# Performance work log

Hardware: AMD Instinct MI355X
Metric: run time of the kernel (lower is better)

Reference implementation:

```python
import jax, jax.numpy as jnp
import numpy as np

N = 100000      # nodes
E = 1600000     # edges
NFEAT = 128
NHID = 32
NHEADS = 8
NCLASS = 40
K = 2           # hop_num
BETA = 0.1      # diffusion teleport weight
ALPHA = 0.2     # leaky relu slope


def setup_inputs() -> dict:
    key = jax.random.key(0)
    ks = jax.random.split(key, 8)
    x = jax.random.normal(ks[0], (N, NFEAT), dtype=jnp.float32)
    edge_index = jax.random.randint(ks[1], (2, E), 0, N, dtype=jnp.int64)
    W = jax.random.normal(ks[2], (NHEADS, NFEAT, NHID), dtype=jnp.float32) * 0.1
    a_src = jax.random.normal(ks[3], (NHEADS, NHID), dtype=jnp.float32) * 0.1
    a_dst = jax.random.normal(ks[4], (NHEADS, NHID), dtype=jnp.float32) * 0.1
    W_out = jax.random.normal(ks[5], (NHEADS * NHID, NCLASS), dtype=jnp.float32) * 0.1
    a_src_out = jax.random.normal(ks[6], (NCLASS,), dtype=jnp.float32) * 0.1
    a_dst_out = jax.random.normal(ks[7], (NCLASS,), dtype=jnp.float32) * 0.1
    return {"x": x, "edge_index": edge_index, "W": W, "a_src": a_src,
            "a_dst": a_dst, "W_out": W_out, "a_src_out": a_src_out,
            "a_dst_out": a_dst_out}


def _khop_attention(h0, src, dst, a_s, a_d):
    """One sparse k-hop attention head. h0: [N, D] transformed features."""
    s = h0 @ a_s            # [N]
    t = h0 @ a_d            # [N]
    e = jax.nn.leaky_relu(s[src] + t[dst], ALPHA)          # [E]
    # numerically stable per-destination softmax over incoming edges
    m = jax.ops.segment_max(e, dst, num_segments=N)        # [N]
    m = jnp.where(jnp.isfinite(m), m, 0.0)                 # empty segments -> -inf
    p = jnp.exp(e - m[dst])                                # [E]
    denom = jax.ops.segment_sum(p, dst, num_segments=N) + 1e-16
    w = p / denom[dst]                                     # [E] attention coeffs
    # k-hop decaying diffusion: feat <- (1-beta)*A_att feat + beta*h0
    feat = h0
    for _ in range(K):
        msg = jax.ops.segment_sum(w[:, None] * feat[src], dst, num_segments=N)
        feat = (1.0 - BETA) * msg + BETA * h0
    return feat


def reference(x, edge_index, W, a_src, a_dst, W_out, a_src_out, a_dst_out):
    src, dst = edge_index[0], edge_index[1]
    # multi-head layer (concat=True -> elu per head, concat along features)
    heads = [jax.nn.elu(_khop_attention(x @ W[i], src, dst, a_src[i], a_dst[i]))
             for i in range(NHEADS)]
    h = jnp.concatenate(heads, axis=1)                     # [N, NHEADS*NHID]
    # output attention layer (concat=False -> raw output)
    out = _khop_attention(h @ W_out, src, dst, a_src_out, a_dst_out)  # [N, NCLASS]
    return jax.nn.log_softmax(jax.nn.elu(out), axis=1)
```

## Files before the change

kernel.cpp:

```cpp
#include <hip/hip_runtime.h>
#include <hip/hip_fp16.h>
#include <stdint.h>

#define NN      100000
#define EE      1600000
#define NFEATC  128
#define NHIDC   32
#define NHEADSC 8
#define NCLASSC 40
#define FDIM    256
#define NBLK    ((NN+255)/256)

typedef unsigned short u16;
typedef __attribute__((ext_vector_type(8))) short bf16x8;
typedef __attribute__((ext_vector_type(4))) float f32x4;

__device__ __forceinline__ float b2f(u16 u){ union{uint32_t i; float f;} v; v.i=((uint32_t)u)<<16; return v.f; }
__device__ __forceinline__ float lof(uint32_t u){ union{uint32_t i; float f;} v; v.i=u<<16; return v.f; }
__device__ __forceinline__ float hif(uint32_t u){ union{uint32_t i; float f;} v; v.i=u&0xFFFF0000u; return v.f; }
__device__ __forceinline__ u16 f2b(float f){ union{float f; uint32_t i;} v; v.f=f; uint32_t x=v.i; return (u16)((x + 0x7FFFu + ((x>>16)&1u))>>16); }
__device__ __forceinline__ uint32_t pack2(float a, float b){ return (uint32_t)f2b(a) | ((uint32_t)f2b(b)<<16); }
__device__ __forceinline__ float lrelu(float e){ return e > 0.f ? e : 0.2f*e; }

__global__ __launch_bounds__(256) void k_transposeW(const float* __restrict__ W, u16* __restrict__ Wt){
  int i = blockIdx.x*256 + threadIdx.x;
  if (i >= FDIM*NFEATC) return;
  int c = i >> 7, k = i & 127;
  int head = c >> 5, hid = c & 31;
  Wt[c*NFEATC + k] = f2b(W[head*(NFEATC*NHIDC) + k*NHIDC + hid]);
}

__global__ __launch_bounds__(256) void k_gemm1_mfma(const float* __restrict__ x, const u16* __restrict__ Wt,
                                                    u16* __restrict__ h0){
  int w = threadIdx.x >> 6, lane = threadIdx.x & 63;
  int nt = blockIdx.x;
  int m = lane & 15, q = lane >> 4;
  int row = nt*16 + m;
  int c0 = w*64;
  const float* xrow = x + (size_t)row*NFEATC;
  f32x4 acc0 = {0.f,0.f,0.f,0.f}, acc1 = {0.f,0.f,0.f,0.f};
  f32x4 acc2 = {0.f,0.f,0.f,0.f}, acc3 = {0.f,0.f,0.f,0.f};
  #pragma unroll
  for (int kk=0; kk<NFEATC; kk+=32){
    int ko = kk + q*8;
    float4 xa = *(const float4*)(xrow + ko);
    float4 xb = *(const float4*)(xrow + ko + 4);
    bf16x8 a;
    a[0]=(short)f2b(xa.x); a[1]=(short)f2b(xa.y); a[2]=(short)f2b(xa.z); a[3]=(short)f2b(xa.w);
    a[4]=(short)f2b(xb.x); a[5]=(short)f2b(xb.y); a[6]=(short)f2b(xb.z); a[7]=(short)f2b(xb.w);
    bf16x8 b0 = *(const bf16x8*)(Wt + (size_t)(c0 +  0 + m)*NFEATC + ko);
    bf16x8 b1 = *(const bf16x8*)(Wt + (size_t)(c0 + 16 + m)*NFEATC + ko);
    bf16x8 b2 = *(const bf16x8*)(Wt + (size_t)(c0 + 32 + m)*NFEATC + ko);
    bf16x8 b3 = *(const bf16x8*)(Wt + (size_t)(c0 + 48 + m)*NFEATC + ko);
    acc0 = __builtin_amdgcn_mfma_f32_16x16x32_bf16(a, b0, acc0, 0,0,0);
    acc1 = __builtin_amdgcn_mfma_f32_16x16x32_bf16(a, b1, acc1, 0,0,0);
    acc2 = __builtin_amdgcn_mfma_f32_16x16x32_bf16(a, b2, acc2, 0,0,0);
    acc3 = __builtin_amdgcn_mfma_f32_16x16x32_bf16(a, b3, acc3, 0,0,0);
  }
  #pragma unroll
  for (int r=0; r<4; r++){
    size_t base = (size_t)(nt*16 + q*4 + r)*FDIM + c0 + m;
    h0[base +  0] = f2b(acc0[r]);
    h0[base + 16] = f2b(acc1[r]);
    h0[base + 32] = f2b(acc2[r]);
    h0[base + 48] = f2b(acc3[r]);
  }
}

__global__ __launch_bounds__(256) void k_st(const u16* __restrict__ h0, const float* __restrict__ a_src,
                                            const float* __restrict__ a_dst, u16* __restrict__ s,
                                            u16* __restrict__ t_){
  int i = blockIdx.x*256 + threadIdx.x;
  if (i >= NN*NHEADSC) return;
  int n = i>>3, head = i&7;
  const u16* hp = h0 + (size_t)n*FDIM + head*NHIDC;
  const float* ap = a_src + head*NHIDC;
  const float* bp = a_dst + head*NHIDC;
  float ss=0.f, tt=0.f;
  #pragma unroll
  for (int j=0;j<NHIDC;j++){
    float h = b2f(hp[j]);
    ss = fmaf(h, ap[j], ss); tt = fmaf(h, bp[j], tt);
  }
  s[i]=f2b(ss); t_[i]=f2b(tt);
}

__global__ __launch_bounds__(256) void k_zero(int* __restrict__ p, int n){
  int i = blockIdx.x*256 + threadIdx.x;
  if (i < n) p[i] = 0;
}
__global__ __launch_bounds__(256) void k_zero_f(float* __restrict__ p, int n){
  int i = blockIdx.x*256 + threadIdx.x;
  if (i < n) p[i] = 0.f;
}
__global__ __launch_bounds__(256) void k_count(const int* __restrict__ dst, int* __restrict__ counts){
  int e = blockIdx.x*256 + threadIdx.x;
  if (e < EE) atomicAdd(&counts[dst[e]], 1);
}
__global__ __launch_bounds__(256) void k_blocksum(const int* __restrict__ counts, int* __restrict__ bsum){
  __shared__ int wsum[4];
  int b = blockIdx.x, t = threadIdx.x;
  int i = b*256 + t;
  int v = (i < NN) ? counts[i] : 0;
  #pragma unroll
  for (int off=32; off; off>>=1) v += __shfl_xor(v, off);
  if ((t & 63) == 0) wsum[t>>6] = v;
  __syncthreads();
  if (t == 0) bsum[b] = wsum[0]+wsum[1]+wsum[2]+wsum[3];
}
__global__ __launch_bounds__(512) void k_scan_bsum(const int* __restrict__ bsum, int* __restrict__ boff){
  __shared__ int lds[512];
  int t = threadIdx.x;
  int v = (t < NBLK) ? bsum[t] : 0;
  lds[t] = v; __syncthreads();
  for (int off=1; off<512; off<<=1){
    int u = (t>=off) ? lds[t-off] : 0;
    __syncthreads();
    lds[t] += u;
    __syncthreads();
  }
  if (t < NBLK) boff[t] = lds[t] - v;
}
__global__ __launch_bounds__(256) void k_scan_final(const int* __restrict__ counts, const int* __restrict__ boff,
                                                    int* __restrict__ row_start){
  __shared__ int lds[256];
  int b = blockIdx.x, t = threadIdx.x;
  int i = b*256 + t;
  int v = (i < NN) ? counts[i] : 0;
  lds[t] = v; __syncthreads();
  for (int off=1; off<256; off<<=1){
    int u = (t>=off) ? lds[t-off] : 0;
    __syncthreads();
    lds[t] += u;
    __syncthreads();
  }
  if (i < NN) row_start[i] = boff[b] + lds[t] - v;
  if (b == 0 && t == 0) row_start[NN] = EE;
}
__global__ __launch_bounds__(256) void k_scatter(const int* __restrict__ src, const int* __restrict__ dst,
                                                 const int* __restrict__ row_start, int* __restrict__ fill,
                                                 int* __restrict__ csr_src){
  int e = blockIdx.x*256 + threadIdx.x;
  if (e >= EE) return;
  int d = dst[e];
  int pos = row_start[d] + atomicAdd(&fill[d], 1);
  csr_src[pos] = src[e];
}

__global__ __launch_bounds__(256) void k_att(const u16* __restrict__ s, const u16* __restrict__ t_,
                                             const int* __restrict__ row_start, const int* __restrict__ csr_src,
                                             u16* __restrict__ p_all, __half* __restrict__ scale){
  int i = blockIdx.x*256 + threadIdx.x;
  if (i >= NN*NHEADSC) return;
  int n = i>>3, head = i&7;
  int beg = row_start[n], end = row_start[n+1];
  float tn = b2f(t_[i]);
  float d0=0.f,d1=0.f,d2=0.f,d3=0.f;
  int pos = beg;
  for (; pos+4<=end; pos+=4){
    int u0=csr_src[pos], u1=csr_src[pos+1], u2=csr_src[pos+2], u3=csr_src[pos+3];
    float e0=lrelu(b2f(s[u0*NHEADSC+head])+tn);
    float e1=lrelu(b2f(s[u1*NHEADSC+head])+tn);
    float e2=lrelu(b2f(s[u2*NHEADSC+head])+tn);
    float e3=lrelu(b2f(s[u3*NHEADSC+head])+tn);
    u16 p0=f2b(__expf(e0)), p1=f2b(__expf(e1)), p2=f2b(__expf(e2)), p3=f2b(__expf(e3));
    p_all[(size_t)(pos+0)*NHEADSC+head]=p0;
    p_all[(size_t)(pos+1)*NHEADSC+head]=p1;
    p_all[(size_t)(pos+2)*NHEADSC+head]=p2;
    p_all[(size_t)(pos+3)*NHEADSC+head]=p3;
    d0+=b2f(p0); d1+=b2f(p1); d2+=b2f(p2); d3+=b2f(p3);
  }
  for (; pos<end; pos++){
    int u = csr_src[pos];
    float e = lrelu(b2f(s[u*NHEADSC+head])+tn);
    u16 pb = f2b(__expf(e));
    p_all[(size_t)pos*NHEADSC+head]=pb;
    d0 += b2f(pb);
  }
  scale[i] = __float2half(1.0f/(((d0+d1)+(d2+d3)) + 1e-16f));
}

#define ACC8(p, g) \
  a0=fmaf(p,lof(g.x),a0); a1=fmaf(p,hif(g.x),a1); \
  a2=fmaf(p,lof(g.y),a2); a3=fmaf(p,hif(g.y),a3); \
  a4=fmaf(p,lof(g.z),a4); a5=fmaf(p,hif(g.z),a5); \
  a6=fmaf(p,lof(g.w),a6); a7=fmaf(p,hif(g.w),a7);

__global__ __launch_bounds__(256) void k_hop1(const u16* __restrict__ h0, const u16* __restrict__ p_all,
                                              const __half* __restrict__ scale, const int* __restrict__ row_start,
                                              const int* __restrict__ csr_src, u16* __restrict__ featA){
  int wv = threadIdx.x >> 6, l = threadIdx.x & 63;
  int n = blockIdx.x*4 + wv;
  int half = l >> 5, sl = l & 31;
  int cg = 8*sl;
  int head = sl >> 2;
  float sc_ = __half2float(scale[n*NHEADSC + head]);
  int beg = row_start[n], end = row_start[n+1];
  float a0=0.f,a1=0.f,a2=0.f,a3=0.f,a4=0.f,a5=0.f,a6=0.f,a7=0.f;
  int pos = beg;
  for (; pos+8<=end; pos+=8){
    int e0=csr_src[pos+0+half], e1=csr_src[pos+2+half], e2=csr_src[pos+4+half], e3=csr_src[pos+6+half];
    float p0=b2f(p_all[(size_t)(pos+0+half)*NHEADSC+head]);
    float p1=b2f(p_all[(size_t)(pos+2+half)*NHEADSC+head]);
    float p2=b2f(p_all[(size_t)(pos+4+half)*NHEADSC+head]);
    float p3=b2f(p_all[(size_t)(pos+6+half)*NHEADSC+head]);
    uint4 g0 = *(const uint4*)(h0 + (size_t)e0*FDIM + cg);
    uint4 g1 = *(const uint4*)(h0 + (size_t)e1*FDIM + cg);
    uint4 g2 = *(const uint4*)(h0 + (size_t)e2*FDIM + cg);
    uint4 g3 = *(const uint4*)(h0 + (size_t)e3*FDIM + cg);
    ACC8(p0, g0) ACC8(p1, g1) ACC8(p2, g2) ACC8(p3, g3)
  }
  for (; pos+2<=end; pos+=2){
    int e = csr_src[pos+half];
    float p = b2f(p_all[(size_t)(pos+half)*NHEADSC+head]);
    uint4 g = *(const uint4*)(h0 + (size_t)e*FDIM + cg);
    ACC8(p, g)
  }
  if (pos < end && half == 0){
    int e = csr_src[pos];
    float p = b2f(p_all[(size_t)pos*NHEADSC+head]);
    uint4 g = *(const uint4*)(h0 + (size_t)e*FDIM + cg);
    ACC8(p, g)
  }
  a0 += __shfl_xor(a0, 32); a1 += __shfl_xor(a1, 32);
  a2 += __shfl_xor(a2, 32); a3 += __shfl_xor(a3, 32);
  a4 += __shfl_xor(a4, 32); a5 += __shfl_xor(a5, 32);
  a6 += __shfl_xor(a6, 32); a7 += __shfl_xor(a7, 32);
  if (half == 0){
    uint4 hu = *(const uint4*)(h0 + (size_t)n*FDIM + cg);
    float r0 = 0.9f*sc_*a0 + 0.1f*lof(hu.x);
    float r1 = 0.9f*sc_*a1 + 0.1f*hif(hu.x);
    float r2 = 0.9f*sc_*a2 + 0.1f*lof(hu.y);
    float r3 = 0.9f*sc_*a3 + 0.1f*hif(hu.y);
    float r4 = 0.9f*sc_*a4 + 0.1f*lof(hu.z);
    float r5 = 0.9f*sc_*a5 + 0.1f*hif(hu.z);
    float r6 = 0.9f*sc_*a6 + 0.1f*lof(hu.w);
    float r7 = 0.9f*sc_*a7 + 0.1f*hif(hu.w);
    uint4 o;
    o.x = pack2(r0,r1); o.y = pack2(r2,r3); o.z = pack2(r4,r5); o.w = pack2(r6,r7);
    *(uint4*)(featA + (size_t)n*FDIM + cg) = o;
  }
}

__global__ __launch_bounds__(256) void k_hop2(const u16* __restrict__ featA, const u16* __restrict__ h0,
                                              const u16* __restrict__ p_all, const __half* __restrict__ scale,
                                              const int* __restrict__ row_start, const int* __restrict__ csr_src,
                                              const float* __restrict__ W_out, float* __restrict__ out0){
  __shared__ float hs[4][FDIM+4];
  int wv = threadIdx.x >> 6, l = threadIdx.x & 63;
  int n = blockIdx.x*4 + wv;
  int half = l >> 5, sl = l & 31;
  int cg = 8*sl;
  int head = sl >> 2;
  float sc_ = __half2float(scale[n*NHEADSC + head]);
  int beg = row_start[n], end = row_start[n+1];
  float a0=0.f,a1=0.f,a2=0.f,a3=0.f,a4=0.f,a5=0.f,a6=0.f,a7=0.f;
  int pos = beg;
  for (; pos+8<=end; pos+=8){
    int e0=csr_src[pos+0+half], e1=csr_src[pos+2+half], e2=csr_src[pos+4+half], e3=csr_src[pos+6+half];
    float p0=b2f(p_all[(size_t)(pos+0+half)*NHEADSC+head]);
    float p1=b2f(p_all[(size_t)(pos+2+half)*NHEADSC+head]);
    float p2=b2f(p_all[(size_t)(pos+4+half)*NHEADSC+head]);
    float p3=b2f(p_all[(size_t)(pos+6+half)*NHEADSC+head]);
    uint4 g0 = *(const uint4*)(featA + (size_t)e0*FDIM + cg);
    uint4 g1 = *(const uint4*)(featA + (size_t)e1*FDIM + cg);
    uint4 g2 = *(const uint4*)(featA + (size_t)e2*FDIM + cg);
    uint4 g3 = *(const uint4*)(featA + (size_t)e3*FDIM + cg);
    ACC8(p0, g0) ACC8(p1, g1) ACC8(p2, g2) ACC8(p3, g3)
  }
  for (; pos+2<=end; pos+=2){
    int e = csr_src[pos+half];
    float p = b2f(p_all[(size_t)(pos+half)*NHEADSC+head]);
    uint4 g = *(const uint4*)(featA + (size_t)e*FDIM + cg);
    ACC8(p, g)
  }
  if (pos < end && half == 0){
    int e = csr_src[pos];
    float p = b2f(p_all[(size_t)pos*NHEADSC+head]);
    uint4 g = *(const uint4*)(featA + (size_t)e*FDIM + cg);
    ACC8(p, g)
  }
  a0 += __shfl_xor(a0, 32); a1 += __shfl_xor(a1, 32);
  a2 += __shfl_xor(a2, 32); a3 += __shfl_xor(a3, 32);
  a4 += __shfl_xor(a4, 32); a5 += __shfl_xor(a5, 32);
  a6 += __shfl_xor(a6, 32); a7 += __shfl_xor(a7, 32);
  if (half == 0){
    uint4 hu = *(const uint4*)(h0 + (size_t)n*FDIM + cg);
    float r0 = 0.9f*sc_*a0 + 0.1f*lof(hu.x);
    float r1 = 0.9f*sc_*a1 + 0.1f*hif(hu.x);
    float r2 = 0.9f*sc_*a2 + 0.1f*lof(hu.y);
    float r3 = 0.9f*sc_*a3 + 0.1f*hif(hu.y);
    float r4 = 0.9f*sc_*a4 + 0.1f*lof(hu.z);
    float r5 = 0.9f*sc_*a5 + 0.1f*hif(hu.z);
    float r6 = 0.9f*sc_*a6 + 0.1f*lof(hu.w);
    float r7 = 0.9f*sc_*a7 + 0.1f*hif(hu.w);
    hs[wv][cg  ] = r0 > 0.f ? r0 : (__expf(r0)-1.0f);
    hs[wv][cg+1] = r1 > 0.f ? r1 : (__expf(r1)-1.0f);
    hs[wv][cg+2] = r2 > 0.f ? r2 : (__expf(r2)-1.0f);
    hs[wv][cg+3] = r3 > 0.f ? r3 : (__expf(r3)-1.0f);
    hs[wv][cg+4] = r4 > 0.f ? r4 : (__expf(r4)-1.0f);
    hs[wv][cg+5] = r5 > 0.f ? r5 : (__expf(r5)-1.0f);
    hs[wv][cg+6] = r6 > 0.f ? r6 : (__expf(r6)-1.0f);
    hs[wv][cg+7] = r7 > 0.f ? r7 : (__expf(r7)-1.0f);
  }
  __syncthreads();
  int t = threadIdx.x;
  if (t < 4*NCLASSC){
    int node = t/NCLASSC, c = t%NCLASSC;
    const float* hv = hs[node];
    const float* wp = W_out + c;
    float o = 0.f;
    #pragma unroll 8
    for (int k=0;k<FDIM;k++) o = fmaf(hv[k], wp[(size_t)k*NCLASSC], o);
    out0[(size_t)(blockIdx.x*4+node)*NCLASSC + c] = o;
  }
}

__global__ __launch_bounds__(256) void k_st_out(const float* __restrict__ out0, const float* __restrict__ a_s,
                                                const float* __restrict__ a_d, float* __restrict__ s,
                                                float* __restrict__ t_){
  int n = blockIdx.x*256 + threadIdx.x;
  if (n >= NN) return;
  const float* r = out0 + (size_t)n*NCLASSC;
  float ss=0.f, tt=0.f;
  for (int c=0;c<NCLASSC;c++){ float v=r[c]; ss=fmaf(v,a_s[c],ss); tt=fmaf(v,a_d[c],tt); }
  s[n]=ss; t_[n]=tt;
}

__global__ __launch_bounds__(256) void k_att_out(const float* __restrict__ s, const float* __restrict__ t_,
                                                 const int* __restrict__ row_start, const int* __restrict__ csr_src,
                                                 float* __restrict__ p_out, float* __restrict__ scale_out){
  int n = blockIdx.x*256 + threadIdx.x;
  if (n >= NN) return;
  int beg = row_start[n], end = row_start[n+1];
  float tn = t_[n];
  float d0=0.f,d1=0.f,d2=0.f,d3=0.f;
  int pos = beg;
  for (; pos+4<=end; pos+=4){
    int u0=csr_src[pos], u1=csr_src[pos+1], u2=csr_src[pos+2], u3=csr_src[pos+3];
    float p0=__expf(lrelu(s[u0]+tn));
    float p1=__expf(lrelu(s[u1]+tn));
    float p2=__expf(lrelu(s[u2]+tn));
    float p3=__expf(lrelu(s[u3]+tn));
    p_out[pos]=p0; p_out[pos+1]=p1; p_out[pos+2]=p2; p_out[pos+3]=p3;
    d0+=p0; d1+=p1; d2+=p2; d3+=p3;
  }
  for (; pos<end; pos++){
    float p = __expf(lrelu(s[csr_src[pos]]+tn));
    p_out[pos] = p;
    d0 += p;
  }
  scale_out[n] = 1.0f/(((d0+d1)+(d2+d3)) + 1e-16f);
}

__global__ __launch_bounds__(64) void k_hop1_out(const float* __restrict__ out0, const float* __restrict__ p_out,
                                                 const float* __restrict__ scale_out, const int* __restrict__ row_start,
                                                 const int* __restrict__ csr_src, u16* __restrict__ outA){
  int n = blockIdx.x, t = threadIdx.x;
  float sc_ = scale_out[n];
  int beg = row_start[n], end = row_start[n+1];
  int tc = (t < NCLASSC) ? t : 0;
  float a0=0.f,a1=0.f,a2=0.f,a3=0.f;
  int pos = beg;
  for (; pos+4<=end; pos+=4){
    int u0=csr_src[pos], u1=csr_src[pos+1], u2=csr_src[pos+2], u3=csr_src[pos+3];
    float p0=p_out[pos], p1=p_out[pos+1], p2=p_out[pos+2], p3=p_out[pos+3];
    float f0=out0[(size_t)u0*NCLASSC+tc];
    float f1=out0[(size_t)u1*NCLASSC+tc];
    float f2=out0[(size_t)u2*NCLASSC+tc];
    float f3=out0[(size_t)u3*NCLASSC+tc];
    a0=fmaf(p0,f0,a0); a1=fmaf(p1,f1,a1); a2=fmaf(p2,f2,a2); a3=fmaf(p3,f3,a3);
  }
  for (; pos<end; pos++){
    a0=fmaf(p_out[pos], out0[(size_t)csr_src[pos]*NCLASSC+tc], a0);
  }
  if (t < NCLASSC){
    float res = 0.9f*sc_*((a0+a1)+(a2+a3)) + 0.1f*out0[(size_t)n*NCLASSC + t];
    outA[(size_t)n*NCLASSC + t] = f2b(res);
  }
}

__global__ __launch_bounds__(64) void k_hop2_out_final(const u16* __restrict__ outA, const float* __restrict__ out0,
                                                       const float* __restrict__ p_out, const float* __restrict__ scale_out,
                                                       const int* __restrict__ row_start, const int* __restrict__ csr_src,
                                                       float* __restrict__ out){
  int n = blockIdx.x, t = threadIdx.x;
  float sc_ = scale_out[n];
  int beg = row_start[n], end = row_start[n+1];
  int tc = (t < NCLASSC) ? t : 0;
  float a0=0.f,a1=0.f,a2=0.f,a3=0.f;
  int pos = beg;
  for (; pos+4<=end; pos+=4){
    int u0=csr_src[pos], u1=csr_src[pos+1], u2=csr_src[pos+2], u3=csr_src[pos+3];
    float p0=p_out[pos], p1=p_out[pos+1], p2=p_out[pos+2], p3=p_out[pos+3];
    float f0=b2f(outA[(size_t)u0*NCLASSC+tc]);
    float f1=b2f(outA[(size_t)u1*NCLASSC+tc]);
    float f2=b2f(outA[(size_t)u2*NCLASSC+tc]);
    float f3=b2f(outA[(size_t)u3*NCLASSC+tc]);
    a0=fmaf(p0,f0,a0); a1=fmaf(p1,f1,a1); a2=fmaf(p2,f2,a2); a3=fmaf(p3,f3,a3);
  }
  for (; pos<end; pos++){
    a0=fmaf(p_out[pos], b2f(outA[(size_t)csr_src[pos]*NCLASSC+tc]), a0);
  }
  float v = -1e30f;
  if (t < NCLASSC){
    float res = 0.9f*sc_*((a0+a1)+(a2+a3)) + 0.1f*out0[(size_t)n*NCLASSC + t];
    v = res > 0.f ? res : (__expf(res)-1.0f);
  }
  float m = v;
  #pragma unroll
  for (int off=32; off; off>>=1) m = fmaxf(m, __shfl_xor(m, off));
  float ex = (t < NCLASSC) ? __expf(v - m) : 0.f;
  float ssum = ex;
  #pragma unroll
  for (int off=32; off; off>>=1) ssum += __shfl_xor(ssum, off);
  if (t < NCLASSC) out[(size_t)n*NCLASSC + t] = v - m - __logf(ssum);
}

extern "C" void kernel_launch(void* const* d_in, const int* in_sizes, int n_in,
                              void* d_out, int out_size, void* d_ws, size_t ws_size,
                              hipStream_t stream){
  const float* x        = (const float*)d_in[0];
  const int*   ei       = (const int*)d_in[1];
  const float* W        = (const float*)d_in[2];
  const float* a_src    = (const float*)d_in[3];
  const float* a_dst    = (const float*)d_in[4];
  const float* W_out    = (const float*)d_in[5];
  const float* a_src_o  = (const float*)d_in[6];
  const float* a_dst_o  = (const float*)d_in[7];
  float* out            = (float*)d_out;
  const int* e_src = ei;
  const int* e_dst = ei + EE;

  char* ws = (char*)d_ws;
  size_t off = 0;
  auto alloc = [&](size_t bytes)->char*{ char* p = ws + off; off += (bytes + 255) & ~(size_t)255; return p; };

  u16*    h0        = (u16*)   alloc((size_t)NN*FDIM*2);
  u16*    featA     = (u16*)   alloc((size_t)NN*FDIM*2);
  float*  out0      = (float*) alloc((size_t)NN*NCLASSC*4);
  int*    csr_src   = (int*)   alloc((size_t)EE*4);
  int*    row_start = (int*)   alloc((size_t)(NN+1)*4);
  char*   regS      =          alloc((size_t)NN*NHEADSC*2*2);
  u16*    p_all     = (u16*)   alloc((size_t)EE*NHEADSC*2);
  __half* scale     = (__half*)alloc((size_t)NN*NHEADSC*2);
  int*    counts    = (int*)   alloc((size_t)NN*4);
  int*    bsum      = (int*)   alloc((size_t)NBLK*4);
  int*    boff      = (int*)   alloc((size_t)NBLK*4);
  u16*    Wt        = (u16*)   alloc((size_t)FDIM*NFEATC*2);

  u16*   s         = (u16*)regS;
  u16*   t_        = (u16*)(regS + (size_t)NN*NHEADSC*2);
  float* s_out     = (float*)regS;
  float* t_out     = s_out + NN;
  float* scale_out = t_out + NN;
  u16*   outA      = (u16*)featA;
  float* p_out     = (float*)p_all;

  k_transposeW<<<(FDIM*NFEATC+255)/256, 256, 0, stream>>>(W, Wt);
  k_gemm1_mfma<<<NN/16, 256, 0, stream>>>(x, Wt, h0);
  k_st<<<(NN*NHEADSC+255)/256, 256, 0, stream>>>(h0, a_src, a_dst, s, t_);

  k_zero<<<(NN+255)/256, 256, 0, stream>>>(counts, NN);
  k_count<<<(EE+255)/256, 256, 0, stream>>>(e_dst, counts);
  k_blocksum<<<NBLK, 256, 0, stream>>>(counts, bsum);
  k_scan_bsum<<<1, 512, 0, stream>>>(bsum, boff);
  k_scan_final<<<NBLK, 256, 0, stream>>>(counts, boff, row_start);
  k_zero<<<(NN+255)/256, 256, 0, stream>>>(counts, NN);
  k_scatter<<<(EE+255)/256, 256, 0, stream>>>(e_src, e_dst, row_start, counts, csr_src);

  k_att<<<(NN*NHEADSC+255)/256, 256, 0, stream>>>(s, t_, row_start, csr_src, p_all, scale);
  k_hop1<<<NN/4, 256, 0, stream>>>(h0, p_all, scale, row_start, csr_src, featA);
  k_hop2<<<NN/4, 256, 0, stream>>>(featA, h0, p_all, scale, row_start, csr_src, W_out, out0);

  k_st_out<<<(NN+255)/256, 256, 0, stream>>>(out0, a_src_o, a_dst_o, s_out, t_out);
  k_att_out<<<(NN+255)/256, 256, 0, stream>>>(s_out, t_out, row_start, csr_src, p_out, scale_out);
  k_hop1_out<<<NN, 64, 0, stream>>>(out0, p_out, scale_out, row_start, csr_src, outA);
  k_hop2_out_final<<<NN, 64, 0, stream>>>(outA, out0, p_out, scale_out, row_start, csr_src, out);
}
```

Before: 845.5 us.

## Fuse attention softmax into hop kernels and recompute edge weights on the fly

Removes the separate attention kernels and the per-edge probability buffer. Each hop kernel now gathers s[src], recomputes the exp-leaky-relu weight, and accumulates the softmax denominator alongside the feature sum. Edge indices are software-prefetched one iteration ahead, and the remainder loops are replaced by masked lanes. W_out is pre-transposed so the dense output projection can use float4 loads. This cuts the writes and re-reads of p_all, at the cost of doing the exp twice per edge (once in each hop) plus extra small gathers of s.

```diff
diff --git a/kernel.cpp b/kernel.cpp
--- a/kernel.cpp
+++ b/kernel.cpp
@@ -28,6 +28,13 @@
   int c = i >> 7, k = i & 127;
   int head = c >> 5, hid = c & 31;
   Wt[c*NFEATC + k] = f2b(W[head*(NFEATC*NHIDC) + k*NHIDC + hid]);
+}
+
+__global__ __launch_bounds__(256) void k_transposeWout(const float* __restrict__ W_out, float* __restrict__ Wo_t){
+  int i = blockIdx.x*256 + threadIdx.x;
+  if (i >= FDIM*NCLASSC) return;
+  int c = i / FDIM, k = i % FDIM;
+  Wo_t[i] = W_out[(size_t)k*NCLASSC + c];
 }
 
 __global__ __launch_bounds__(256) void k_gemm1_mfma(const float* __restrict__ x, const u16* __restrict__ Wt,
@@ -89,10 +96,6 @@
   int i = blockIdx.x*256 + threadIdx.x;
   if (i < n) p[i] = 0;
 }
-__global__ __launch_bounds__(256) void k_zero_f(float* __restrict__ p, int n){
-  int i = blockIdx.x*256 + threadIdx.x;
-  if (i < n) p[i] = 0.f;
-}
 __global__ __launch_bounds__(256) void k_count(const int* __restrict__ dst, int* __restrict__ counts){
   int e = blockIdx.x*256 + threadIdx.x;
   if (e < EE) atomicAdd(&counts[dst[e]], 1);
@@ -147,95 +150,64 @@
   csr_src[pos] = src[e];
 }
 
-__global__ __launch_bounds__(256) void k_att(const u16* __restrict__ s, const u16* __restrict__ t_,
-                                             const int* __restrict__ row_start, const int* __restrict__ csr_src,
-                                             u16* __restrict__ p_all, __half* __restrict__ scale){
-  int i = blockIdx.x*256 + threadIdx.x;
-  if (i >= NN*NHEADSC) return;
-  int n = i>>3, head = i&7;
-  int beg = row_start[n], end = row_start[n+1];
-  float tn = b2f(t_[i]);
-  float d0=0.f,d1=0.f,d2=0.f,d3=0.f;
-  int pos = beg;
-  for (; pos+4<=end; pos+=4){
-    int u0=csr_src[pos], u1=csr_src[pos+1], u2=csr_src[pos+2], u3=csr_src[pos+3];
-    float e0=lrelu(b2f(s[u0*NHEADSC+head])+tn);
-    float e1=lrelu(b2f(s[u1*NHEADSC+head])+tn);
-    float e2=lrelu(b2f(s[u2*NHEADSC+head])+tn);
-    float e3=lrelu(b2f(s[u3*NHEADSC+head])+tn);
-    u16 p0=f2b(__expf(e0)), p1=f2b(__expf(e1)), p2=f2b(__expf(e2)), p3=f2b(__expf(e3));
-    p_all[(size_t)(pos+0)*NHEADSC+head]=p0;
-    p_all[(size_t)(pos+1)*NHEADSC+head]=p1;
-    p_all[(size_t)(pos+2)*NHEADSC+head]=p2;
-    p_all[(size_t)(pos+3)*NHEADSC+head]=p3;
-    d0+=b2f(p0); d1+=b2f(p1); d2+=b2f(p2); d3+=b2f(p3);
-  }
-  for (; pos<end; pos++){
-    int u = csr_src[pos];
-    float e = lrelu(b2f(s[u*NHEADSC+head])+tn);
-    u16 pb = f2b(__expf(e));
-    p_all[(size_t)pos*NHEADSC+head]=pb;
-    d0 += b2f(pb);
-  }
-  scale[i] = __float2half(1.0f/(((d0+d1)+(d2+d3)) + 1e-16f));
-}
-
 #define ACC8(p, g) \
   a0=fmaf(p,lof(g.x),a0); a1=fmaf(p,hif(g.x),a1); \
   a2=fmaf(p,lof(g.y),a2); a3=fmaf(p,hif(g.y),a3); \
   a4=fmaf(p,lof(g.z),a4); a5=fmaf(p,hif(g.z),a5); \
   a6=fmaf(p,lof(g.w),a6); a7=fmaf(p,hif(g.w),a7);
 
-__global__ __launch_bounds__(256) void k_hop1(const u16* __restrict__ h0, const u16* __restrict__ p_all,
-                                              const __half* __restrict__ scale, const int* __restrict__ row_start,
+__global__ __launch_bounds__(256) void k_hop1(const u16* __restrict__ h0, const u16* __restrict__ s,
+                                              const u16* __restrict__ t_, const int* __restrict__ row_start,
                                               const int* __restrict__ csr_src, u16* __restrict__ featA){
   int wv = threadIdx.x >> 6, l = threadIdx.x & 63;
   int n = blockIdx.x*4 + wv;
   int half = l >> 5, sl = l & 31;
   int cg = 8*sl;
   int head = sl >> 2;
-  float sc_ = __half2float(scale[n*NHEADSC + head]);
+  float tn = b2f(t_[n*NHEADSC + head]);
   int beg = row_start[n], end = row_start[n+1];
-  float a0=0.f,a1=0.f,a2=0.f,a3=0.f,a4=0.f,a5=0.f,a6=0.f,a7=0.f;
-  int pos = beg;
-  for (; pos+8<=end; pos+=8){
-    int e0=csr_src[pos+0+half], e1=csr_src[pos+2+half], e2=csr_src[pos+4+half], e3=csr_src[pos+6+half];
-    float p0=b2f(p_all[(size_t)(pos+0+half)*NHEADSC+head]);
-    float p1=b2f(p_all[(size_t)(pos+2+half)*NHEADSC+head]);
-    float p2=b2f(p_all[(size_t)(pos+4+half)*NHEADSC+head]);
-    float p3=b2f(p_all[(size_t)(pos+6+half)*NHEADSC+head]);
+  float a0=0.f,a1=0.f,a2=0.f,a3=0.f,a4=0.f,a5=0.f,a6=0.f,a7=0.f,den=0.f;
+  int e0,e1,e2,e3;
+  {
+    int v0=beg+half, v1=beg+2+half, v2=beg+4+half, v3=beg+6+half;
+    int c0=csr_src[v0<EE?v0:EE-1], c1=csr_src[v1<EE?v1:EE-1];
+    int c2=csr_src[v2<EE?v2:EE-1], c3=csr_src[v3<EE?v3:EE-1];
+    e0 = v0<end?c0:n; e1 = v1<end?c1:n; e2 = v2<end?c2:n; e3 = v3<end?c3:n;
+  }
+  for (int pos=beg; pos<end; pos+=8){
+    int w0=pos+8+half, w1=pos+10+half, w2=pos+12+half, w3=pos+14+half;
+    int c0=csr_src[w0<EE?w0:EE-1], c1=csr_src[w1<EE?w1:EE-1];
+    int c2=csr_src[w2<EE?w2:EE-1], c3=csr_src[w3<EE?w3:EE-1];
+    float s0=b2f(s[e0*NHEADSC+head]), s1=b2f(s[e1*NHEADSC+head]);
+    float s2=b2f(s[e2*NHEADSC+head]), s3=b2f(s[e3*NHEADSC+head]);
     uint4 g0 = *(const uint4*)(h0 + (size_t)e0*FDIM + cg);
     uint4 g1 = *(const uint4*)(h0 + (size_t)e1*FDIM + cg);
     uint4 g2 = *(const uint4*)(h0 + (size_t)e2*FDIM + cg);
     uint4 g3 = *(const uint4*)(h0 + (size_t)e3*FDIM + cg);
-    ACC8(p0, g0) ACC8(p1, g1) ACC8(p2, g2) ACC8(p3, g3)
-  }
-  for (; pos+2<=end; pos+=2){
-    int e = csr_src[pos+half];
-    float p = b2f(p_all[(size_t)(pos+half)*NHEADSC+head]);
-    uint4 g = *(const uint4*)(h0 + (size_t)e*FDIM + cg);
-    ACC8(p, g)
-  }
-  if (pos < end && half == 0){
-    int e = csr_src[pos];
-    float p = b2f(p_all[(size_t)pos*NHEADSC+head]);
-    uint4 g = *(const uint4*)(h0 + (size_t)e*FDIM + cg);
-    ACC8(p, g)
+    float p0 = (pos+half   < end) ? __expf(lrelu(s0+tn)) : 0.f;
+    float p1 = (pos+2+half < end) ? __expf(lrelu(s1+tn)) : 0.f;
+    float p2 = (pos+4+half < end) ? __expf(lrelu(s2+tn)) : 0.f;
+    float p3 = (pos+6+half < end) ? __expf(lrelu(s3+tn)) : 0.f;
+    den += (p0+p1)+(p2+p3);
+    ACC8(p0,g0) ACC8(p1,g1) ACC8(p2,g2) ACC8(p3,g3)
+    e0 = w0<end?c0:n; e1 = w1<end?c1:n; e2 = w2<end?c2:n; e3 = w3<end?c3:n;
   }
   a0 += __shfl_xor(a0, 32); a1 += __shfl_xor(a1, 32);
   a2 += __shfl_xor(a2, 32); a3 += __shfl_xor(a3, 32);
   a4 += __shfl_xor(a4, 32); a5 += __shfl_xor(a5, 32);
   a6 += __shfl_xor(a6, 32); a7 += __shfl_xor(a7, 32);
+  den += __shfl_xor(den, 32);
+  float sc_ = 0.9f/(den + 1e-16f);
   if (half == 0){
     uint4 hu = *(const uint4*)(h0 + (size_t)n*FDIM + cg);
-    float r0 = 0.9f*sc_*a0 + 0.1f*lof(hu.x);
-    float r1 = 0.9f*sc_*a1 + 0.1f*hif(hu.x);
-    float r2 = 0.9f*sc_*a2 + 0.1f*lof(hu.y);
-    float r3 = 0.9f*sc_*a3 + 0.1f*hif(hu.y);
-    float r4 = 0.9f*sc_*a4 + 0.1f*lof(hu.z);
-    float r5 = 0.9f*sc_*a5 + 0.1f*hif(hu.z);
-    float r6 = 0.9f*sc_*a6 + 0.1f*lof(hu.w);
-    float r7 = 0.9f*sc_*a7 + 0.1f*hif(hu.w);
+    float r0 = sc_*a0 + 0.1f*lof(hu.x);
+    float r1 = sc_*a1 + 0.1f*hif(hu.x);
+    float r2 = sc_*a2 + 0.1f*lof(hu.y);
+    float r3 = sc_*a3 + 0.1f*hif(hu.y);
+    float r4 = sc_*a4 + 0.1f*lof(hu.z);
+    float r5 = sc_*a5 + 0.1f*hif(hu.z);
+    float r6 = sc_*a6 + 0.1f*lof(hu.w);
+    float r7 = sc_*a7 + 0.1f*hif(hu.w);
     uint4 o;
     o.x = pack2(r0,r1); o.y = pack2(r2,r3); o.z = pack2(r4,r5); o.w = pack2(r6,r7);
     *(uint4*)(featA + (size_t)n*FDIM + cg) = o;
@@ -243,76 +215,86 @@
 }
 
 __global__ __launch_bounds__(256) void k_hop2(const u16* __restrict__ featA, const u16* __restrict__ h0,
-                                              const u16* __restrict__ p_all, const __half* __restrict__ scale,
+                                              const u16* __restrict__ s, const u16* __restrict__ t_,
                                               const int* __restrict__ row_start, const int* __restrict__ csr_src,
-                                              const float* __restrict__ W_out, float* __restrict__ out0){
-  __shared__ float hs[4][FDIM+4];
+                                              const float* __restrict__ Wo_t, float* __restrict__ out0){
+  __shared__ __align__(16) float hs[4][FDIM+4];
   int wv = threadIdx.x >> 6, l = threadIdx.x & 63;
   int n = blockIdx.x*4 + wv;
   int half = l >> 5, sl = l & 31;
   int cg = 8*sl;
   int head = sl >> 2;
-  float sc_ = __half2float(scale[n*NHEADSC + head]);
+  float tn = b2f(t_[n*NHEADSC + head]);
   int beg = row_start[n], end = row_start[n+1];
-  float a0=0.f,a1=0.f,a2=0.f,a3=0.f,a4=0.f,a5=0.f,a6=0.f,a7=0.f;
-  int pos = beg;
-  for (; pos+8<=end; pos+=8){
-    int e0=csr_src[pos+0+half], e1=csr_src[pos+2+half], e2=csr_src[pos+4+half], e3=csr_src[pos+6+half];
-    float p0=b2f(p_all[(size_t)(pos+0+half)*NHEADSC+head]);
-    float p1=b2f(p_all[(size_t)(pos+2+half)*NHEADSC+head]);
-    float p2=b2f(p_all[(size_t)(pos+4+half)*NHEADSC+head]);
-    float p3=b2f(p_all[(size_t)(pos+6+half)*NHEADSC+head]);
+  float a0=0.f,a1=0.f,a2=0.f,a3=0.f,a4=0.f,a5=0.f,a6=0.f,a7=0.f,den=0.f;
+  int e0,e1,e2,e3;
+  {
+    int v0=beg+half, v1=beg+2+half, v2=beg+4+half, v3=beg+6+half;
+    int c0=csr_src[v0<EE?v0:EE-1], c1=csr_src[v1<EE?v1:EE-1];
+    int c2=csr_src[v2<EE?v2:EE-1], c3=csr_src[v3<EE?v3:EE-1];
+    e0 = v0<end?c0:n; e1 = v1<end?c1:n; e2 = v2<end?c2:n; e3 = v3<end?c3:n;
+  }
+  for (int pos=beg; pos<end; pos+=8){
+    int w0=pos+8+half, w1=pos+10+half, w2=pos+12+half, w3=pos+14+half;
+    int c0=csr_src[w0<EE?w0:EE-1], c1=csr_src[w1<EE?w1:EE-1];
+    int c2=csr_src[w2<EE?w2:EE-1], c3=csr_src[w3<EE?w3:EE-1];
+    float s0=b2f(s[e0*NHEADSC+head]), s1=b2f(s[e1*NHEADSC+head]);
+    float s2=b2f(s[e2*NHEADSC+head]), s3=b2f(s[e3*NHEADSC+head]);
     uint4 g0 = *(const uint4*)(featA + (size_t)e0*FDIM + cg);
     uint4 g1 = *(const uint4*)(featA + (size_t)e1*FDIM + cg);
     uint4 g2 = *(const uint4*)(featA + (size_t)e2*FDIM + cg);
     uint4 g3 = *(const uint4*)(featA + (size_t)e3*FDIM + cg);
-    ACC8(p0, g0) ACC8(p1, g1) ACC8(p2, g2) ACC8(p3, g3)
-  }
-  for (; pos+2<=end; pos+=2){
-    int e = csr_src[pos+half];
-    float p = b2f(p_all[(size_t)(pos+half)*NHEADSC+head]);
-    uint4 g = *(const uint4*)(featA + (size_t)e*FDIM + cg);
-    ACC8(p, g)
-  }
-  if (pos < end && half == 0){
-    int e = csr_src[pos];
-    float p = b2f(p_all[(size_t)pos*NHEADSC+head]);
-    uint4 g = *(const uint4*)(featA + (size_t)e*FDIM + cg);
-    ACC8(p, g)
+    float p0 = (pos+half   < end) ? __expf(lrelu(s0+tn)) : 0.f;
+    float p1 = (pos+2+half < end) ? __expf(lrelu(s1+tn)) : 0.f;
+    float p2 = (pos+4+half < end) ? __expf(lrelu(s2+tn)) : 0.f;
+    float p3 = (pos+6+half < end) ? __expf(lrelu(s3+tn)) : 0.f;
+    den += (p0+p1)+(p2+p3);
+    ACC8(p0,g0) ACC8(p1,g1) ACC8(p2,g2) ACC8(p3,g3)
+    e0 = w0<end?c0:n; e1 = w1<end?c1:n; e2 = w2<end?c2:n; e3 = w3<end?c3:n;
   }
   a0 += __shfl_xor(a0, 32); a1 += __shfl_xor(a1, 32);
   a2 += __shfl_xor(a2, 32); a3 += __shfl_xor(a3, 32);
   a4 += __shfl_xor(a4, 32); a5 += __shfl_xor(a5, 32);
   a6 += __shfl_xor(a6, 32); a7 += __shfl_xor(a7, 32);
+  den += __shfl_xor(den, 32);
+  float sc_ = 0.9f/(den + 1e-16f);
   if (half == 0){
     uint4 hu = *(const uint4*)(h0 + (size_t)n*FDIM + cg);
-    float r0 = 0.9f*sc_*a0 + 0.1f*lof(hu.x);
-    float r1 = 0.9f*sc_*a1 + 0.1f*hif(hu.x);
-    float r2 = 0.9f*sc_*a2 + 0.1f*lof(hu.y);
-    float r3 = 0.9f*sc_*a3 + 0.1f*hif(hu.y);
-    float r4 = 0.9f*sc_*a4 + 0.1f*lof(hu.z);
-    float r5 = 0.9f*sc_*a5 + 0.1f*hif(hu.z);
-    float r6 = 0.9f*sc_*a6 + 0.1f*lof(hu.w);
-    float r7 = 0.9f*sc_*a7 + 0.1f*hif(hu.w);
-    hs[wv][cg  ] = r0 > 0.f ? r0 : (__expf(r0)-1.0f);
-    hs[wv][cg+1] = r1 > 0.f ? r1 : (__expf(r1)-1.0f);
-    hs[wv][cg+2] = r2 > 0.f ? r2 : (__expf(r2)-1.0f);
-    hs[wv][cg+3] = r3 > 0.f ? r3 : (__expf(r3)-1.0f);
-    hs[wv][cg+4] = r4 > 0.f ? r4 : (__expf(r4)-1.0f);
-    hs[wv][cg+5] = r5 > 0.f ? r5 : (__expf(r5)-1.0f);
-    hs[wv][cg+6] = r6 > 0.f ? r6 : (__expf(r6)-1.0f);
-    hs[wv][cg+7] = r7 > 0.f ? r7 : (__expf(r7)-1.0f);
+    float r0 = sc_*a0 + 0.1f*lof(hu.x);
+    float r1 = sc_*a1 + 0.1f*hif(hu.x);
+    float r2 = sc_*a2 + 0.1f*lof(hu.y);
+    float r3 = sc_*a3 + 0.1f*hif(hu.y);
+    float r4 = sc_*a4 + 0.1f*lof(hu.z);
+    float r5 = sc_*a5 + 0.1f*hif(hu.z);
+    float r6 = sc_*a6 + 0.1f*lof(hu.w);
+    float r7 = sc_*a7 + 0.1f*hif(hu.w);
+    float4 ha, hb;
+    ha.x = r0 > 0.f ? r0 : (__expf(r0)-1.0f);
+    ha.y = r1 > 0.f ? r1 : (__expf(r1)-1.0f);
+    ha.z = r2 > 0.f ? r2 : (__expf(r2)-1.0f);
+    ha.w = r3 > 0.f ? r3 : (__expf(r3)-1.0f);
+    hb.x = r4 > 0.f ? r4 : (__expf(r4)-1.0f);
+    hb.y = r5 > 0.f ? r5 : (__expf(r5)-1.0f);
+    hb.z = r6 > 0.f ? r6 : (__expf(r6)-1.0f);
+    hb.w = r7 > 0.f ? r7 : (__expf(r7)-1.0f);
+    *(float4*)&hs[wv][cg  ] = ha;
+    *(float4*)&hs[wv][cg+4] = hb;
   }
   __syncthreads();
   int t = threadIdx.x;
   if (t < 4*NCLASSC){
     int node = t/NCLASSC, c = t%NCLASSC;
     const float* hv = hs[node];
-    const float* wp = W_out + c;
-    float o = 0.f;
+    const float* wt = Wo_t + (size_t)c*FDIM;
+    float o0=0.f,o1=0.f,o2=0.f,o3=0.f;
     #pragma unroll 8
-    for (int k=0;k<FDIM;k++) o = fmaf(hv[k], wp[(size_t)k*NCLASSC], o);
-    out0[(size_t)(blockIdx.x*4+node)*NCLASSC + c] = o;
+    for (int k=0;k<FDIM;k+=4){
+      float4 h4 = *(const float4*)(hv + k);
+      float4 w4 = *(const float4*)(wt + k);
+      o0=fmaf(h4.x,w4.x,o0); o1=fmaf(h4.y,w4.y,o1);
+      o2=fmaf(h4.z,w4.z,o2); o3=fmaf(h4.w,w4.w,o3);
+    }
+    out0[(size_t)(blockIdx.x*4+node)*NCLASSC + c] = (o0+o1)+(o2+o3);
   }
 }
 
@@ -327,84 +309,78 @@
   s[n]=ss; t_[n]=tt;
 }
 
-__global__ __launch_bounds__(256) void k_att_out(const float* __restrict__ s, const float* __restrict__ t_,
-                                                 const int* __restrict__ row_start, const int* __restrict__ csr_src,
-                                                 float* __restrict__ p_out, float* __restrict__ scale_out){
-  int n = blockIdx.x*256 + threadIdx.x;
-  if (n >= NN) return;
-  int beg = row_start[n], end = row_start[n+1];
-  float tn = t_[n];
-  float d0=0.f,d1=0.f,d2=0.f,d3=0.f;
-  int pos = beg;
-  for (; pos+4<=end; pos+=4){
-    int u0=csr_src[pos], u1=csr_src[pos+1], u2=csr_src[pos+2], u3=csr_src[pos+3];
-    float p0=__expf(lrelu(s[u0]+tn));
-    float p1=__expf(lrelu(s[u1]+tn));
-    float p2=__expf(lrelu(s[u2]+tn));
-    float p3=__expf(lrelu(s[u3]+tn));
-    p_out[pos]=p0; p_out[pos+1]=p1; p_out[pos+2]=p2; p_out[pos+3]=p3;
-    d0+=p0; d1+=p1; d2+=p2; d3+=p3;
-  }
-  for (; pos<end; pos++){
-    float p = __expf(lrelu(s[csr_src[pos]]+tn));
-    p_out[pos] = p;
-    d0 += p;
-  }
-  scale_out[n] = 1.0f/(((d0+d1)+(d2+d3)) + 1e-16f);
-}
-
-__global__ __launch_bounds__(64) void k_hop1_out(const float* __restrict__ out0, const float* __restrict__ p_out,
-                                                 const float* __restrict__ scale_out, const int* __restrict__ row_start,
+__global__ __launch_bounds__(64) void k_hop1_out(const float* __restrict__ out0, const float* __restrict__ s_out,
+                                                 const float* __restrict__ t_out, const int* __restrict__ row_start,
                                                  const int* __restrict__ csr_src, u16* __restrict__ outA){
   int n = blockIdx.x, t = threadIdx.x;
-  float sc_ = scale_out[n];
+  float tn = t_out[n];
   int beg = row_start[n], end = row_start[n+1];
   int tc = (t < NCLASSC) ? t : 0;
-  float a0=0.f,a1=0.f,a2=0.f,a3=0.f;
-  int pos = beg;
-  for (; pos+4<=end; pos+=4){
-    int u0=csr_src[pos], u1=csr_src[pos+1], u2=csr_src[pos+2], u3=csr_src[pos+3];
-    float p0=p_out[pos], p1=p_out[pos+1], p2=p_out[pos+2], p3=p_out[pos+3];
-    float f0=out0[(size_t)u0*NCLASSC+tc];
-    float f1=out0[(size_t)u1*NCLASSC+tc];
-    float f2=out0[(size_t)u2*NCLASSC+tc];
-    float f3=out0[(size_t)u3*NCLASSC+tc];
+  float a0=0.f,a1=0.f,a2=0.f,a3=0.f,den=0.f;
+  int u0,u1,u2,u3;
+  {
+    int v1=beg+1, v2=beg+2, v3=beg+3;
+    int c0=csr_src[beg<EE?beg:EE-1], c1=csr_src[v1<EE?v1:EE-1];
+    int c2=csr_src[v2<EE?v2:EE-1], c3=csr_src[v3<EE?v3:EE-1];
+    u0 = beg<end?c0:n; u1 = v1<end?c1:n; u2 = v2<end?c2:n; u3 = v3<end?c3:n;
+  }
+  for (int pos=beg; pos<end; pos+=4){
+    int w0=pos+4, w1=pos+5, w2=pos+6, w3=pos+7;
+    int c0=csr_src[w0<EE?w0:EE-1], c1=csr_src[w1<EE?w1:EE-1];
+    int c2=csr_src[w2<EE?w2:EE-1], c3=csr_src[w3<EE?w3:EE-1];
+    float sv0=s_out[u0], sv1=s_out[u1], sv2=s_out[u2], sv3=s_out[u3];
+    float f0=out0[(size_t)u0*NCLASSC+tc], f1=out0[(size_t)u1*NCLASSC+tc];
+    float f2=out0[(size_t)u2*NCLASSC+tc], f3=out0[(size_t)u3*NCLASSC+tc];
+    float p0 = __expf(lrelu(sv0+tn));
+    float p1 = (pos+1<end)?__expf(lrelu(sv1+tn)):0.f;
+    float p2 = (pos+2<end)?__expf(lrelu(sv2+tn)):0.f;
+    float p3 = (pos+3<end)?__expf(lrelu(sv3+tn)):0.f;
+    den += (p0+p1)+(p2+p3);
     a0=fmaf(p0,f0,a0); a1=fmaf(p1,f1,a1); a2=fmaf(p2,f2,a2); a3=fmaf(p3,f3,a3);
-  }
-  for (; pos<end; pos++){
-    a0=fmaf(p_out[pos], out0[(size_t)csr_src[pos]*NCLASSC+tc], a0);
-  }
+    u0 = w0<end?c0:n; u1 = w1<end?c1:n; u2 = w2<end?c2:n; u3 = w3<end?c3:n;
+  }
+  float inv = 0.9f/(den + 1e-16f);
   if (t < NCLASSC){
-    float res = 0.9f*sc_*((a0+a1)+(a2+a3)) + 0.1f*out0[(size_t)n*NCLASSC + t];
+    float res = inv*((a0+a1)+(a2+a3)) + 0.1f*out0[(size_t)n*NCLASSC + t];
     outA[(size_t)n*NCLASSC + t] = f2b(res);
   }
 }
 
 __global__ __launch_bounds__(64) void k_hop2_out_final(const u16* __restrict__ outA, const float* __restrict__ out0,
-                                                       const float* __restrict__ p_out, const float* __restrict__ scale_out,
+                                                       const float* __restrict__ s_out, const float* __restrict__ t_out,
                                                        const int* __restrict__ row_start, const int* __restrict__ csr_src,
                                                        float* __restrict__ out){
   int n = blockIdx.x, t = threadIdx.x;
-  float sc_ = scale_out[n];
+  float tn = t_out[n];
   int beg = row_start[n], end = row_start[n+1];
   int tc = (t < NCLASSC) ? t : 0;
-  float a0=0.f,a1=0.f,a2=0.f,a3=0.f;
-  int pos = beg;
-  for (; pos+4<=end; pos+=4){
-    int u0=csr_src[pos], u1=csr_src[pos+1], u2=csr_src[pos+2], u3=csr_src[pos+3];
-    float p0=p_out[pos], p1=p_out[pos+1], p2=p_out[pos+2], p3=p_out[pos+3];
-    float f0=b2f(outA[(size_t)u0*NCLASSC+tc]);
-    float f1=b2f(outA[(size_t)u1*NCLASSC+tc]);
-    float f2=b2f(outA[(size_t)u2*NCLASSC+tc]);
-    float f3=b2f(outA[(size_t)u3*NCLASSC+tc]);
+  float a0=0.f,a1=0.f,a2=0.f,a3=0.f,den=0.f;
+  int u0,u1,u2,u3;
+  {
+    int v1=beg+1, v2=beg+2, v3=beg+3;
+    int c0=csr_src[beg<EE?beg:EE-1], c1=csr_src[v1<EE?v1:EE-1];
+    int c2=csr_src[v2<EE?v2:EE-1], c3=csr_src[v3<EE?v3:EE-1];
+    u0 = beg<end?c0:n; u1 = v1<end?c1:n; u2 = v2<end?c2:n; u3 = v3<end?c3:n;
+  }
+  for (int pos=beg; pos<end; pos+=4){
+    int w0=pos+4, w1=pos+5, w2=pos+6, w3=pos+7;
+    int c0=csr_src[w0<EE?w0:EE-1], c1=csr_src[w1<EE?w1:EE-1];
+    int c2=csr_src[w2<EE?w2:EE-1], c3=csr_src[w3<EE?w3:EE-1];
+    float sv0=s_out[u0], sv1=s_out[u1], sv2=s_out[u2], sv3=s_out[u3];
+    float f0=b2f(outA[(size_t)u0*NCLASSC+tc]), f1=b2f(outA[(size_t)u1*NCLASSC+tc]);
+    float f2=b2f(outA[(size_t)u2*NCLASSC+tc]), f3=b2f(outA[(size_t)u3*NCLASSC+tc]);
+    float p0 = __expf(lrelu(sv0+tn));
+    float p1 = (pos+1<end)?__expf(lrelu(sv1+tn)):0.f;
+    float p2 = (pos+2<end)?__expf(lrelu(sv2+tn)):0.f;
+    float p3 = (pos+3<end)?__expf(lrelu(sv3+tn)):0.f;
+    den += (p0+p1)+(p2+p3);
     a0=fmaf(p0,f0,a0); a1=fmaf(p1,f1,a1); a2=fmaf(p2,f2,a2); a3=fmaf(p3,f3,a3);
-  }
-  for (; pos<end; pos++){
-    a0=fmaf(p_out[pos], b2f(outA[(size_t)csr_src[pos]*NCLASSC+tc]), a0);
-  }
+    u0 = w0<end?c0:n; u1 = w1<end?c1:n; u2 = w2<end?c2:n; u3 = w3<end?c3:n;
+  }
+  float inv = 0.9f/(den + 1e-16f);
   float v = -1e30f;
   if (t < NCLASSC){
-    float res = 0.9f*sc_*((a0+a1)+(a2+a3)) + 0.1f*out0[(size_t)n*NCLASSC + t];
+    float res = inv*((a0+a1)+(a2+a3)) + 0.1f*out0[(size_t)n*NCLASSC + t];
     v = res > 0.f ? res : (__expf(res)-1.0f);
   }
   float m = v;
@@ -442,22 +418,20 @@
   int*    csr_src   = (int*)   alloc((size_t)EE*4);
   int*    row_start = (int*)   alloc((size_t)(NN+1)*4);
   char*   regS      =          alloc((size_t)NN*NHEADSC*2*2);
-  u16*    p_all     = (u16*)   alloc((size_t)EE*NHEADSC*2);
-  __half* scale     = (__half*)alloc((size_t)NN*NHEADSC*2);
   int*    counts    = (int*)   alloc((size_t)NN*4);
   int*    bsum      = (int*)   alloc((size_t)NBLK*4);
   int*    boff      = (int*)   alloc((size_t)NBLK*4);
   u16*    Wt        = (u16*)   alloc((size_t)FDIM*NFEATC*2);
+  float*  Wo_t      = (float*) alloc((size_t)FDIM*NCLASSC*4);
 
   u16*   s         = (u16*)regS;
   u16*   t_        = (u16*)(regS + (size_t)NN*NHEADSC*2);
   float* s_out     = (float*)regS;
   float* t_out     = s_out + NN;
-  float* scale_out = t_out + NN;
   u16*   outA      = (u16*)featA;
-  float* p_out     = (float*)p_all;
 
   k_transposeW<<<(FDIM*NFEATC+255)/256, 256, 0, stream>>>(W, Wt);
+  k_transposeWout<<<(FDIM*NCLASSC+255)/256, 256, 0, stream>>>(W_out, Wo_t);
   k_gemm1_mfma<<<NN/16, 256, 0, stream>>>(x, Wt, h0);
   k_st<<<(NN*NHEADSC+255)/256, 256, 0, stream>>>(h0, a_src, a_dst, s, t_);
 
@@ -469,12 +443,10 @@
   k_zero<<<(NN+255)/256, 256, 0, stream>>>(counts, NN);
   k_scatter<<<(EE+255)/256, 256, 0, stream>>>(e_src, e_dst, row_start, counts, csr_src);
 
-  k_att<<<(NN*NHEADSC+255)/256, 256, 0, stream>>>(s, t_, row_start, csr_src, p_all, scale);
-  k_hop1<<<NN/4, 256, 0, stream>>>(h0, p_all, scale, row_start, csr_src, featA);
-  k_hop2<<<NN/4, 256, 0, stream>>>(featA, h0, p_all, scale, row_start, csr_src, W_out, out0);
+  k_hop1<<<NN/4, 256, 0, stream>>>(h0, s, t_, row_start, csr_src, featA);
+  k_hop2<<<NN/4, 256, 0, stream>>>(featA, h0, s, t_, row_start, csr_src, Wo_t, out0);
 
   k_st_out<<<(NN+255)/256, 256, 0, stream>>>(out0, a_src_o, a_dst_o, s_out, t_out);
-  k_att_out<<<(NN+255)/256, 256, 0, stream>>>(s_out, t_out, row_start, csr_src, p_out, scale_out);
-  k_hop1_out<<<NN, 64, 0, stream>>>(out0, p_out, scale_out, row_start, csr_src, outA);
-  k_hop2_out_final<<<NN, 64, 0, stream>>>(outA, out0, p_out, scale_out, row_start, csr_src, out);
-}
+  k_hop1_out<<<NN, 64, 0, stream>>>(out0, s_out, t_out, row_start, csr_src, outA);
+  k_hop2_out_final<<<NN, 64, 0, stream>>>(outA, out0, s_out, t_out, row_start, csr_src, out);
+}
```

After: 1.162 ms. 37.5% more time.
